# Performance work log

Hardware: AMD Instinct MI355X
Metric: run time of the kernel (lower is better)

## Reference

```python
import jax, jax.numpy as jnp
import numpy as np

N, P, C, S, H, CLS = 32, 16, 256, 128, 4, 3000
DH = C // H
EPS = 1e-5


def setup_inputs() -> dict:
    key = jax.random.key(0)
    ks = jax.random.split(key, 8)
    sh = (N, P, C, S)
    return {
        "t_f": jax.random.normal(ks[0], sh, jnp.float32),
        "t_s": jax.random.normal(ks[1], sh, jnp.float32),
        "t_l": jax.random.normal(ks[2], sh, jnp.float32),
        # grouped 1x1 conv weights, one [out_ch, in_ch] matrix per part
        "decay_w": jax.random.normal(ks[3], (P, C, 3 * C), jnp.float32) * 0.02,
        "qkv_w": jax.random.normal(ks[4], (P, 3 * C, C), jnp.float32) * 0.02,
        "out_w": jax.random.normal(ks[5], (P, C, C), jnp.float32) * 0.02,
        # per-part BatchNorm1d affine params
        "gamma": jnp.ones((P, C), jnp.float32),
        "beta": jnp.zeros((P, C), jnp.float32),
        # classifier fc: [in_planes, class_num] (broadcast over parts)
        "fc": jax.random.normal(ks[6], (C, CLS), jnp.float32) * 0.02,
    }


def reference(t_f, t_s, t_l, decay_w, qkv_w, out_w, gamma, beta, fc):
    n, p, c, s = t_f.shape
    h, dh = H, DH
    scale = dh ** -0.5

    # decay_c: grouped 1x1 conv, 3c -> c per part
    x_cat = jnp.concatenate([t_f, t_s, t_l], axis=2)            # [n,p,3c,s]
    t_all = jnp.einsum('npis,poi->npos', x_cat, decay_w)        # [n,p,c,s]

    # Attention.to_qkv: grouped 1x1 conv, c -> 3c per part
    qkv = jnp.einsum('npcs,pqc->npqs', t_all, qkv_w)            # [n,p,3c,s]
    qkv = qkv.reshape(n, p, 3, h, dh, s).transpose(2, 0, 3, 1, 4, 5)  # [3,n,h,p,dh,s]
    q, k, v = qkv[0], qkv[1], qkv[2]

    # frame-frame attention per (head, part): [n,h,p,s,s]
    dots = jnp.einsum('nhpcs,nhpct->nhpst', q, k) * scale
    attn = jax.nn.softmax(dots, axis=-1)

    o = jnp.einsum('nhpst,nhpct->nhpcs', attn, v)               # [n,h,p,dh,s]
    o = o.transpose(0, 2, 1, 3, 4).reshape(n, p, c, s)          # [n,p,c,s]
    o = jnp.einsum('npcs,poc->npos', o, out_w)                  # to_out grouped conv

    # residual + max over frames
    wpv = (o + t_all).max(axis=-1)                              # [n,p,c]

    # select_topk_part (topk_num == 1 forced by squeeze(2) in torch code):
    # argmax over frames of column-summed attention, gather that frame of t_f, sum heads
    idx = jnp.argmax(attn.sum(axis=-2), axis=-1)                # [n,h,p]
    ib = jnp.broadcast_to(idx[:, :, :, None, None], (n, h, p, c, 1))
    sel = jnp.take_along_axis(t_f[:, None], ib, axis=-1)[..., 0]  # [n,h,p,c]
    sel = sel.sum(axis=1)                                       # [n,p,c]

    # per-part BatchNorm1d in training mode (batch statistics over n)
    mean = wpv.mean(axis=0)                                     # [p,c]
    var = wpv.var(axis=0)                                       # biased, as torch BN
    pf = (wpv - mean) / jnp.sqrt(var + EPS) * gamma + beta      # [n,p,c]

    cls = jnp.einsum('npc,ck->npk', pf, fc)                     # [n,p,class_num]
    return cls, wpv.transpose(1, 0, 2), sel.transpose(1, 0, 2)
```

## Files before the change

### kernel.cpp

```cpp
#include <hip/hip_runtime.h>
#include <math.h>

#define N_ 32
#define P_ 16
#define C_ 256
#define S_ 128
#define H_ 4
#define CLS_ 3000

typedef __attribute__((ext_vector_type(4))) float f4v;
typedef __attribute__((ext_vector_type(4))) float f32x4;
typedef __attribute__((ext_vector_type(8))) short short8;
typedef __attribute__((ext_vector_type(4))) unsigned short us4;

__device__ __forceinline__ unsigned short f2bf(float x){
    unsigned u = __float_as_uint(x);
    u += 0x7fffu + ((u >> 16) & 1u);
    return (unsigned short)(u >> 16);
}
__device__ __forceinline__ float bf2f(unsigned short h){
    return __uint_as_float(((unsigned)h) << 16);
}

typedef __attribute__((address_space(1))) const unsigned int gu32_t;
typedef __attribute__((address_space(3))) unsigned int lu32_t;
__device__ __forceinline__ void gload16(const void* g, void* l){
    __builtin_amdgcn_global_load_lds((gu32_t*)g, (lu32_t*)l, 16, 0, 0);
}

__global__ void wsplit(const float* __restrict__ dw, const float* __restrict__ qw,
                       const float* __restrict__ ow,
                       unsigned short* __restrict__ wdh, unsigned short* __restrict__ wdl,
                       unsigned short* __restrict__ wqh, unsigned short* __restrict__ wql,
                       unsigned short* __restrict__ woh){
    int i = blockIdx.x * 256 + threadIdx.x;
    int stride = gridDim.x * 256;
    for (; i < 3145728; i += stride){
        float a = dw[i]; unsigned short h = f2bf(a);
        wdh[i] = h; wdl[i] = f2bf(a - bf2f(h));
        float b = qw[i]; unsigned short h2 = f2bf(b);
        wqh[i] = h2; wql[i] = f2bf(b - bf2f(h2));
        if (i < 1048576) woh[i] = f2bf(ow[i]);
    }
}

__global__ __launch_bounds__(256) void fct_kernel(const float* __restrict__ fc,
                                                  unsigned short* __restrict__ fcT){
    int n = blockIdx.x * 256 + threadIdx.x;
    if (n < CLS_){
        for (int c = 0; c < 256; ++c) fcT[(size_t)n * 256 + c] = f2bf(fc[(size_t)c * CLS_ + n]);
    } else {
        for (int c = 0; c < 256; ++c) fcT[(size_t)n * 256 + c] = 0;
    }
}

__global__ __launch_bounds__(256) void gemm0t(
    const float* __restrict__ t_f, const float* __restrict__ t_s,
    const float* __restrict__ t_l,
    const unsigned short* __restrict__ Whi, const unsigned short* __restrict__ Wlo,
    unsigned short* __restrict__ outH, unsigned short* __restrict__ outL,
    int n0, int cnp)
{
    __shared__ unsigned short sm[24576];
    float* Tf = (float*)sm;
    unsigned short* AhL = sm + 8192;
    unsigned short* AlL = sm + 12288;
    unsigned short* BhL = sm + 16384;
    unsigned short* BlL = sm + 20480;
    unsigned short* Ep  = sm;

    const int id = blockIdx.x;
    const int xcd = id & 7;
    const int r = id >> 3;
    const int ppl = r / (cnp * 2);
    const int rr = r % (cnp * 2);
    const int n_l = rr >> 1;
    const int o_t = rr & 1;
    const int p = xcd * 2 + ppl;
    const int np_l = n_l * 16 + p;
    const int o0 = o_t * 128;
    const size_t np_g = (size_t)(n0 + n_l) * 16 + p;

    const int tid = threadIdx.x;
    const int w = tid >> 6, l = tid & 63;
    const int lr = l & 15, lg = l >> 4;
    const int ws0 = (w & 1) * 64, wo0 = (w >> 1) * 64;
    const int s2 = tid & 127, khalf = tid >> 7;

    const unsigned short* Wp_h = Whi + ((size_t)p * 256 + o0) * 768;
    const unsigned short* Wp_l = Wlo + ((size_t)p * 256 + o0) * 768;

    f32x4 acc[4][4];
#pragma unroll
    for (int i = 0; i < 4; ++i)
#pragma unroll
        for (int j = 0; j < 4; ++j) acc[i][j] = (f32x4){0.f, 0.f, 0.f, 0.f};

    for (int k0 = 0; k0 < 768; k0 += 32){
        const int t = k0 >> 8;
        const float* src = (t == 0) ? t_f : ((t == 1) ? t_s : t_l);
        const float* xbase = src + (np_g * 256 + (k0 & 255)) * 128;
#pragma unroll
        for (int it = 0; it < 4; ++it){
            int lin = (w * 4 + it) * 64 + l;
            gload16(xbase + lin * 4, Tf + lin * 4);
        }
#pragma unroll
        for (int it = 0; it < 2; ++it){
            int lin = (w * 2 + it) * 64 + l;
            int row = lin >> 2, ch = lin & 3;
            int sk = ((ch ^ ((row >> 1) & 3)) << 3);
            gload16(Wp_h + (size_t)row * 768 + k0 + sk, BhL + lin * 8);
            gload16(Wp_l + (size_t)row * 768 + k0 + sk, BlL + lin * 8);
        }
        __syncthreads();
        {
            short8 h0, h1, l0, l1;
#pragma unroll
            for (int j = 0; j < 8; ++j){
                float v = Tf[(khalf * 16 + j) * 128 + s2];
                unsigned short hh = f2bf(v);
                h0[j] = (short)hh; l0[j] = (short)f2bf(v - bf2f(hh));
            }
#pragma unroll
            for (int j = 0; j < 8; ++j){
                float v = Tf[(khalf * 16 + 8 + j) * 128 + s2];
                unsigned short hh = f2bf(v);
                h1[j] = (short)hh; l1[j] = (short)f2bf(v - bf2f(hh));
            }
            int sb = (s2 >> 1) & 3;
            int c0 = (khalf * 2) ^ sb, c1 = (khalf * 2 + 1) ^ sb;
            *(short8*)(AhL + s2 * 32 + c0 * 8) = h0;
            *(short8*)(AhL + s2 * 32 + c1 * 8) = h1;
            *(short8*)(AlL + s2 * 32 + c0 * 8) = l0;
            *(short8*)(AlL + s2 * 32 + c1 * 8) = l1;
        }
        __syncthreads();
        short8 ah[4], al[4];
#pragma unroll
        for (int sf = 0; sf < 4; ++sf){
            int row = ws0 + sf * 16 + lr;
            int cof = (lg ^ ((row >> 1) & 3)) << 3;
            ah[sf] = *(const short8*)(AhL + row * 32 + cof);
            al[sf] = *(const short8*)(AlL + row * 32 + cof);
        }
#pragma unroll
        for (int of = 0; of < 4; ++of){
            int row = wo0 + of * 16 + lr;
            int cof = (lg ^ ((row >> 1) & 3)) << 3;
            short8 bh = *(const short8*)(BhL + row * 32 + cof);
            short8 bl = *(const short8*)(BlL + row * 32 + cof);
#pragma unroll
            for (int sf = 0; sf < 4; ++sf){
                acc[sf][of] = __builtin_amdgcn_mfma_f32_16x16x32_bf16(ah[sf], bh, acc[sf][of], 0, 0, 0);
                acc[sf][of] = __builtin_amdgcn_mfma_f32_16x16x32_bf16(ah[sf], bl, acc[sf][of], 0, 0, 0);
                acc[sf][of] = __builtin_amdgcn_mfma_f32_16x16x32_bf16(al[sf], bh, acc[sf][of], 0, 0, 0);
            }
        }
        __syncthreads();
    }

#pragma unroll
    for (int plane = 0; plane < 2; ++plane){
#pragma unroll
        for (int sf = 0; sf < 4; ++sf)
#pragma unroll
            for (int of = 0; of < 4; ++of){
                int col = wo0 + of * 16 + lr;
#pragma unroll
                for (int r2 = 0; r2 < 4; ++r2){
                    int row = ws0 + sf * 16 + lg * 4 + r2;
                    float v = acc[sf][of][r2];
                    unsigned short hh = f2bf(v);
                    unsigned short q = plane ? f2bf(v - bf2f(hh)) : hh;
                    Ep[row * 136 + col] = q;
                }
            }
        __syncthreads();
        unsigned short* dst = plane ? outL : outH;
#pragma unroll
        for (int it = 0; it < 8; ++it){
            int idx = tid + 256 * it;
            int row = idx >> 4, seg = (idx & 15) * 8;
            *(short8*)(dst + (size_t)np_l * 128 * 256 + (size_t)row * 256 + o0 + seg) =
                *(const short8*)(Ep + row * 136 + seg);
        }
        __syncthreads();
    }
}

template<int KEXT, int APITCH, int ND, int MODE, int OPITCH>
__global__ __launch_bounds__(256) void gemm3(
    const unsigned short* __restrict__ Ah_g, const unsigned short* __restrict__ Al_g,
    const unsigned short* __restrict__ Whi, const unsigned short* __restrict__ Wlo,
    const unsigned short* __restrict__ resH, const unsigned short* __restrict__ resL,
    unsigned short* __restrict__ outH, unsigned short* __restrict__ outL,
    float* __restrict__ outF, int n0, int cnp)
{
    constexpr int T3 = (MODE == 2) ? 0 : 1;
    constexpr int OB = ND / 128;
    __shared__ unsigned short sm[(T3 ? 4 : 2) * 128 * 64];
    unsigned short* AhL = sm;
    unsigned short* BhL = sm + 8192;
    unsigned short* AlL = T3 ? (sm + 16384) : sm;
    unsigned short* BlL = T3 ? (sm + 24576) : sm;
    unsigned short* Ep = sm;
    __shared__ float cmax[2][2][64];

    const int id = blockIdx.x;
    const int xcd = id & 7;
    const int r = id >> 3;
    const int ppl = r / (cnp * OB);
    const int rr = r % (cnp * OB);
    const int n_l = rr / OB;
    const int o_t = rr % OB;
    const int p = xcd * 2 + ppl;
    const int np_l = n_l * 16 + p;
    const int o0 = o_t * 128;

    const int tid = threadIdx.x;
    const int w = tid >> 6, l = tid & 63;
    const int lr = l & 15, lg = l >> 4;
    const int ws0 = (w & 1) * 64, wo0 = (w >> 1) * 64;
    const size_t aBase = (size_t)np_l * 128 * APITCH;
    const unsigned short* Wp_h = Whi + ((size_t)p * ND + o0) * KEXT;
    const unsigned short* Wp_l = T3 ? (Wlo + ((size_t)p * ND + o0) * KEXT) : Wp_h;

    f32x4 acc[4][4];
#pragma unroll
    for (int i = 0; i < 4; ++i)
#pragma unroll
        for (int j = 0; j < 4; ++j) acc[i][j] = (f32x4){0.f, 0.f, 0.f, 0.f};

    for (int k0 = 0; k0 < KEXT; k0 += 64){
#pragma unroll
        for (int it = 0; it < 4; ++it){
            int slot = w * 4 + it;
            int lin = slot * 64 + l;
            int row = lin >> 3, chnk = lin & 7;
            int sk = ((chnk ^ (row & 7)) << 3);
            unsigned short* ldst = sm + slot * 512;
            const unsigned short* ga = Ah_g + aBase + (size_t)row * APITCH + k0 + sk;
            gload16(ga, ldst);
            const unsigned short* gb = Wp_h + (size_t)row * KEXT + k0 + sk;
            gload16(gb, ldst + 8192);
            if (T3){
                gload16(Al_g + aBase + (size_t)row * APITCH + k0 + sk, ldst + 16384);
                gload16(Wp_l + (size_t)row * KEXT + k0 + sk, ldst + 24576);
            }
        }
        __syncthreads();
#pragma unroll
        for (int ks = 0; ks < 2; ++ks){
            short8 ah[4], al[4];
#pragma unroll
            for (int sf = 0; sf < 4; ++sf){
                int row = ws0 + sf * 16 + lr;
                int cof = ((ks * 4 + lg) ^ (row & 7)) << 3;
                ah[sf] = *(const short8*)(AhL + row * 64 + cof);
                if (T3) al[sf] = *(const short8*)(AlL + row * 64 + cof);
            }
#pragma unroll
            for (int of = 0; of < 4; ++of){
                int row = wo0 + of * 16 + lr;
                int cof = ((ks * 4 + lg) ^ (row & 7)) << 3;
                short8 bh = *(const short8*)(BhL + row * 64 + cof);
                short8 bl = bh;
                if (T3) bl = *(const short8*)(BlL + row * 64 + cof);
#pragma unroll
                for (int sf = 0; sf < 4; ++sf){
                    acc[sf][of] = __builtin_amdgcn_mfma_f32_16x16x32_bf16(ah[sf], bh, acc[sf][of], 0, 0, 0);
                    if (T3){
                        acc[sf][of] = __builtin_amdgcn_mfma_f32_16x16x32_bf16(ah[sf], bl, acc[sf][of], 0, 0, 0);
                        acc[sf][of] = __builtin_amdgcn_mfma_f32_16x16x32_bf16(al[sf], bh, acc[sf][of], 0, 0, 0);
                    }
                }
            }
        }
        __syncthreads();
    }

    if (MODE != 2){
#pragma unroll
        for (int plane = 0; plane < 2; ++plane){
#pragma unroll
            for (int sf = 0; sf < 4; ++sf)
#pragma unroll
                for (int of = 0; of < 4; ++of){
                    int col = wo0 + of * 16 + lr;
#pragma unroll
                    for (int r2 = 0; r2 < 4; ++r2){
                        int row = ws0 + sf * 16 + lg * 4 + r2;
                        float v = acc[sf][of][r2];
                        unsigned short hh = f2bf(v);
                        unsigned short q = plane ? f2bf(v - bf2f(hh)) : hh;
                        Ep[row * 136 + col] = q;
                    }
                }
            __syncthreads();
            unsigned short* dst = plane ? outL : outH;
#pragma unroll
            for (int it = 0; it < 8; ++it){
                int idx = tid + 256 * it;
                int row = idx >> 4, seg = (idx & 15) * 8;
                *(short8*)(dst + (size_t)np_l * 128 * OPITCH + (size_t)row * OPITCH + o0 + seg) =
                    *(const short8*)(Ep + row * 136 + seg);
            }
            __syncthreads();
        }
    } else {
        const int n_g = n0 + n_l;
#pragma unroll
        for (int of = 0; of < 4; ++of){
            int oc = o0 + wo0 + of * 16 + lr;
            float m = -INFINITY;
#pragma unroll
            for (int sf = 0; sf < 4; ++sf){
#pragma unroll
                for (int r2 = 0; r2 < 4; ++r2){
                    int s = ws0 + sf * 16 + lg * 4 + r2;
                    size_t ri = (size_t)np_l * 128 * 256 + (size_t)s * 256 + oc;
                    float v = acc[sf][of][r2] + bf2f(resH[ri]) + bf2f(resL[ri]);
                    m = fmaxf(m, v);
                }
            }
            m = fmaxf(m, __shfl_xor(m, 16));
            m = fmaxf(m, __shfl_xor(m, 32));
            if (l < 16) cmax[w >> 1][w & 1][of * 16 + l] = m;
        }
        __syncthreads();
        if (tid < 128){
            int oh = tid >> 6, col = tid & 63;
            float v = fmaxf(cmax[oh][0][col], cmax[oh][1][col]);
            outF[((size_t)p * N_ + n_g) * C_ + o0 + oh * 64 + col] = v;
        }
    }
}

__global__ __launch_bounds__(256) void attn3(unsigned short* __restrict__ qH,
                                             const unsigned short* __restrict__ qL,
                                             int* __restrict__ idxA, int n0, int cnp){
    __shared__ char smraw[17408 + 34816 + 2048];
    unsigned short* Vs = (unsigned short*)smraw;
    unsigned short* Pm = (unsigned short*)(smraw + 17408);
    float* csW = (float*)(smraw + 17408 + 34816);
    unsigned short* Ot = (unsigned short*)smraw;

    const int id = blockIdx.x;
    const int xcd = id & 7;
    const int r = id >> 3;
    const int ppl = r / (cnp * 4);
    const int rr = r % (cnp * 4);
    const int n_l = rr >> 2, h = rr & 3;
    const int p = xcd * 2 + ppl;
    const int np_l = n_l * 16 + p;
    const int tid = threadIdx.x, w = tid >> 6, l = tid & 63;
    const int lr = l & 15, lg = l >> 4;
    unsigned short* baseH = qH + (size_t)np_l * 128 * 768;
    const unsigned short* baseL = qL + (size_t)np_l * 128 * 768;

#pragma unroll
    for (int it = 0; it < 8; ++it){
        int idx = tid + 256 * it;
        int t = idx >> 4, d4 = (idx & 15) * 4;
        us4 v = *(const us4*)(baseH + (size_t)t * 768 + 512 + h * 64 + d4);
#pragma unroll
        for (int j = 0; j < 4; ++j) Vs[(d4 + j) * 136 + t] = v[j];
    }

    short8 qh[2][2], ql[2][2];
#pragma unroll
    for (int sf = 0; sf < 2; ++sf)
#pragma unroll
        for (int ks = 0; ks < 2; ++ks){
            size_t off = (size_t)(w * 32 + sf * 16 + lr) * 768 + h * 64 + ks * 32 + lg * 8;
            qh[sf][ks] = *(const short8*)(baseH + off);
            ql[sf][ks] = *(const short8*)(baseL + off);
        }

    f32x4 dacc[2][8];
#pragma unroll
    for (int i = 0; i < 2; ++i)
#pragma unroll
        for (int j = 0; j < 8; ++j) dacc[i][j] = (f32x4){0.f, 0.f, 0.f, 0.f};

#pragma unroll
    for (int tf = 0; tf < 8; ++tf){
#pragma unroll
        for (int ks = 0; ks < 2; ++ks){
            size_t off = (size_t)(tf * 16 + lr) * 768 + 256 + h * 64 + ks * 32 + lg * 8;
            short8 kh = *(const short8*)(baseH + off);
            short8 kl = *(const short8*)(baseL + off);
#pragma unroll
            for (int sf = 0; sf < 2; ++sf){
                dacc[sf][tf] = __builtin_amdgcn_mfma_f32_16x16x32_bf16(qh[sf][ks], kh, dacc[sf][tf], 0, 0, 0);
                dacc[sf][tf] = __builtin_amdgcn_mfma_f32_16x16x32_bf16(qh[sf][ks], kl, dacc[sf][tf], 0, 0, 0);
                dacc[sf][tf] = __builtin_amdgcn_mfma_f32_16x16x32_bf16(ql[sf][ks], kh, dacc[sf][tf], 0, 0, 0);
            }
        }
    }

    float csp[8];
#pragma unroll
    for (int tf = 0; tf < 8; ++tf) csp[tf] = 0.f;
#pragma unroll
    for (int sf = 0; sf < 2; ++sf){
#pragma unroll
        for (int r2 = 0; r2 < 4; ++r2){
            float m = -INFINITY;
#pragma unroll
            for (int tf = 0; tf < 8; ++tf) m = fmaxf(m, dacc[sf][tf][r2]);
            m = fmaxf(m, __shfl_xor(m, 1)); m = fmaxf(m, __shfl_xor(m, 2));
            m = fmaxf(m, __shfl_xor(m, 4)); m = fmaxf(m, __shfl_xor(m, 8));
            float e[8]; float sum = 0.f;
#pragma unroll
            for (int tf = 0; tf < 8; ++tf){
                e[tf] = __expf(0.125f * (dacc[sf][tf][r2] - m)); sum += e[tf];
            }
            sum += __shfl_xor(sum, 1); sum += __shfl_xor(sum, 2);
            sum += __shfl_xor(sum, 4); sum += __shfl_xor(sum, 8);
            float inv = 1.f / sum;
            int s = w * 32 + sf * 16 + lg * 4 + r2;
#pragma unroll
            for (int tf = 0; tf < 8; ++tf){
                float pv = e[tf] * inv;
                Pm[s * 136 + tf * 16 + lr] = f2bf(pv);
                csp[tf] += pv;
            }
        }
    }
#pragma unroll
    for (int tf = 0; tf < 8; ++tf){
        float v = csp[tf];
        v += __shfl_xor(v, 16); v += __shfl_xor(v, 32);
        if (l < 16) csW[w * 128 + tf * 16 + l] = v;
    }
    __syncthreads();

    f32x4 oacc[8];
#pragma unroll
    for (int i = 0; i < 8; ++i) oacc[i] = (f32x4){0.f, 0.f, 0.f, 0.f};
#pragma unroll
    for (int ks = 0; ks < 4; ++ks){
        short8 av = *(const short8*)(Vs + (w * 16 + lr) * 136 + ks * 32 + lg * 8);
#pragma unroll
        for (int sf = 0; sf < 8; ++sf){
            short8 bp = *(const short8*)(Pm + (sf * 16 + lr) * 136 + ks * 32 + lg * 8);
            oacc[sf] = __builtin_amdgcn_mfma_f32_16x16x32_bf16(av, bp, oacc[sf], 0, 0, 0);
        }
    }
    __syncthreads();

    if (tid < 64){
        float v0 = csW[tid] + csW[128 + tid] + csW[256 + tid] + csW[384 + tid];
        float v1 = csW[64 + tid] + csW[192 + tid] + csW[320 + tid] + csW[448 + tid];
        float bv; int bi;
        if (v1 > v0){ bv = v1; bi = 64 + tid; } else { bv = v0; bi = tid; }
#pragma unroll
        for (int msk = 1; msk <= 32; msk <<= 1){
            float ov = __shfl_xor(bv, msk); int oi = __shfl_xor(bi, msk);
            if (ov > bv || (ov == bv && oi < bi)){ bv = ov; bi = oi; }
        }
        if (tid == 0){ int n_g = n0 + n_l; idxA[(n_g * H_ + h) * P_ + p] = bi; }
    }

#pragma unroll
    for (int sf = 0; sf < 8; ++sf){
        int s = sf * 16 + lr;
#pragma unroll
        for (int r2 = 0; r2 < 4; ++r2) Ot[s * 72 + w * 16 + lg * 4 + r2] = f2bf(oacc[sf][r2]);
    }
    __syncthreads();
#pragma unroll
    for (int it = 0; it < 4; ++it){
        int idx = tid + 256 * it;
        int s = idx >> 3, d8 = (idx & 7) * 8;
        *(short8*)(baseH + (size_t)s * 768 + h * 64 + d8) = *(const short8*)(Ot + s * 72 + d8);
    }
}

__global__ void bn_stats(const float* __restrict__ wpvT,
                         const float* __restrict__ gamma,
                         const float* __restrict__ beta,
                         float* __restrict__ aArr, float* __restrict__ bArr)
{
    int i = blockIdx.x * blockDim.x + threadIdx.x;
    if (i >= P_ * C_) return;
    int p = i / C_, c = i % C_;
    const float* basep = wpvT + (size_t)p * N_ * C_ + c;
    float su = 0.f, s2 = 0.f;
    for (int n = 0; n < N_; ++n){
        float v = basep[n * C_];
        su += v; s2 += v * v;
    }
    float mean = su * (1.f / N_);
    float var = s2 * (1.f / N_) - mean * mean;
    float rstd = rsqrtf(var + 1e-5f);
    float a = gamma[i] * rstd;
    aArr[i] = a;
    bArr[i] = beta[i] - mean * a;
}

__global__ __launch_bounds__(256) void pf_kernel(const float* __restrict__ wpvT,
                                                 const float* __restrict__ aArr,
                                                 const float* __restrict__ bArr,
                                                 unsigned short* __restrict__ pfb){
    int m = blockIdx.x, c = threadIdx.x;
    int p = m >> 5;
    float v = wpvT[(size_t)m * 256 + c];
    pfb[(size_t)m * 256 + c] = f2bf(v * aArr[p * 256 + c] + bArr[p * 256 + c]);
}

__global__ __launch_bounds__(256) void gemmc(const unsigned short* __restrict__ pfb,
                                             const unsigned short* __restrict__ fcT,
                                             float* __restrict__ cls){
    __shared__ unsigned short sm[2 * 128 * 72];
    unsigned short* AhL = sm;
    unsigned short* BhL = sm + 128 * 72;

    const int tid = threadIdx.x;
    const int w = tid >> 6, l = tid & 63;
    const int lr = l & 15, lg = l >> 4;
    const int ws0 = (w & 1) * 64, wo0 = (w >> 1) * 64;
    const int o0 = blockIdx.x * 128;
    const int m0 = blockIdx.y * 128;

    f32x4 acc[4][4];
#pragma unroll
    for (int i = 0; i < 4; ++i)
#pragma unroll
        for (int j = 0; j < 4; ++j) acc[i][j] = (f32x4){0.f, 0.f, 0.f, 0.f};

    for (int k0 = 0; k0 < 256; k0 += 64){
#pragma unroll
        for (int it = 0; it < 4; ++it){
            int idx = tid + 256 * it;
            int s = idx >> 3, c8 = (idx & 7) * 8;
            *(short8*)(AhL + s * 72 + c8) = *(const short8*)(pfb + (size_t)(m0 + s) * 256 + k0 + c8);
            *(short8*)(BhL + s * 72 + c8) = *(const short8*)(fcT + (size_t)(o0 + s) * 256 + k0 + c8);
        }
        __syncthreads();
#pragma unroll
        for (int ks = 0; ks < 2; ++ks){
            short8 ah[4];
#pragma unroll
            for (int sf = 0; sf < 4; ++sf)
                ah[sf] = *(const short8*)(AhL + (ws0 + sf * 16 + lr) * 72 + ks * 32 + lg * 8);
#pragma unroll
            for (int of = 0; of < 4; ++of){
                short8 bh = *(const short8*)(BhL + (wo0 + of * 16 + lr) * 72 + ks * 32 + lg * 8);
#pragma unroll
                for (int sf = 0; sf < 4; ++sf)
                    acc[sf][of] = __builtin_amdgcn_mfma_f32_16x16x32_bf16(ah[sf], bh, acc[sf][of], 0, 0, 0);
            }
        }
        __syncthreads();
    }
#pragma unroll
    for (int sf = 0; sf < 4; ++sf)
#pragma unroll
        for (int of = 0; of < 4; ++of){
            int oc = o0 + wo0 + of * 16 + lr;
            if (oc < CLS_){
#pragma unroll
                for (int r2 = 0; r2 < 4; ++r2){
                    int m = m0 + ws0 + sf * 16 + lg * 4 + r2;
                    int n = m & 31, p = m >> 5;
                    cls[((size_t)n * 16 + p) * CLS_ + oc] = acc[sf][of][r2];
                }
            }
        }
}

__global__ void sel_kernel(const float* __restrict__ t_f,
                           const int* __restrict__ idxArr,
                           float* __restrict__ selT)
{
    const int np = blockIdx.x;
    const int n = np >> 4, p = np & 15;
    const int c = threadIdx.x;
    float acc = 0.f;
#pragma unroll
    for (int h = 0; h < H_; ++h){
        int s = idxArr[(n * H_ + h) * P_ + p];
        acc += t_f[((size_t)np * C_ + c) * S_ + s];
    }
    selT[((size_t)p * N_ + n) * C_ + c] = acc;
}

extern "C" void kernel_launch(void* const* d_in, const int* in_sizes, int n_in,
                              void* d_out, int out_size, void* d_ws, size_t ws_size,
                              hipStream_t stream)
{
    const float* t_f     = (const float*)d_in[0];
    const float* t_s     = (const float*)d_in[1];
    const float* t_l     = (const float*)d_in[2];
    const float* decay_w = (const float*)d_in[3];
    const float* qkv_w   = (const float*)d_in[4];
    const float* out_w   = (const float*)d_in[5];
    const float* gamma   = (const float*)d_in[6];
    const float* beta    = (const float*)d_in[7];
    const float* fc      = (const float*)d_in[8];
    float* out = (float*)d_out;

    const size_t WD = 3145728, WQ = 3145728, WO = 1048576;
    char* basep = (char*)d_ws;
    unsigned short* wdh = (unsigned short*)basep;
    unsigned short* wdl = wdh + WD;
    unsigned short* wqh = wdl + WD;
    unsigned short* wql = wqh + WQ;
    unsigned short* woh = wql + WQ;
    unsigned short* fcT = woh + WO;
    unsigned short* pfb = fcT + 3072 * 256;
    float* aArr = (float*)(pfb + 512 * 256);
    float* bArr = aArr + P_ * C_;
    int* idxA = (int*)(bArr + P_ * C_);
    char* big = (char*)(idxA + N_ * H_ * P_);
    size_t head = (size_t)(big - basep);
    size_t avail = (ws_size > head) ? (ws_size - head) : 0;
    const size_t per_n = (size_t)16 * 128 * (256 + 768) * 2 * 2;
    int cn = (int)(avail / per_n);
    if (cn < 1) cn = 1;
    if (cn > N_) cn = N_;
    int nch = (N_ + cn - 1) / cn;
    cn = (N_ + nch - 1) / nch;

    unsigned short* tH = (unsigned short*)big;
    unsigned short* tL = tH + (size_t)cn * 16 * 128 * 256;
    unsigned short* qH = tL + (size_t)cn * 16 * 128 * 256;
    unsigned short* qL = qH + (size_t)cn * 16 * 128 * 768;

    float* cls  = out;
    float* wpvT = out + (size_t)N_ * P_ * CLS_;
    float* selT = wpvT + (size_t)P_ * N_ * C_;

    wsplit<<<2048, 256, 0, stream>>>(decay_w, qkv_w, out_w, wdh, wdl, wqh, wql, woh);
    fct_kernel<<<12, 256, 0, stream>>>(fc, fcT);

    for (int n0 = 0; n0 < N_; n0 += cn){
        int c = (N_ - n0 < cn) ? (N_ - n0) : cn;
        int npg = c * 16;
        gemm0t<<<npg * 2, 256, 0, stream>>>(
            t_f, t_s, t_l, wdh, wdl, tH, tL, n0, c);
        gemm3<256, 256, 768, 1, 768><<<npg * 6, 256, 0, stream>>>(
            tH, tL, wqh, wql, nullptr, nullptr, qH, qL, nullptr, n0, c);
        attn3<<<c * 64, 256, 0, stream>>>(qH, qL, idxA, n0, c);
        gemm3<256, 768, 256, 2, 256><<<npg * 2, 256, 0, stream>>>(
            qH, qH, woh, woh, tH, tL, nullptr, nullptr, wpvT, n0, c);
    }
    bn_stats<<<(P_ * C_ + 255) / 256, 256, 0, stream>>>(wpvT, gamma, beta, aArr, bArr);
    pf_kernel<<<512, 256, 0, stream>>>(wpvT, aArr, bArr, pfb);
    gemmc<<<dim3(24, 4), 256, 0, stream>>>(pfb, fcT, cls);
    sel_kernel<<<N_ * P_, 256, 0, stream>>>(t_f, idxA, selT);
}
```

Before: 439.5 us.

## Retile decay GEMM over all outputs and halve K-step in gemm3

The first GEMM (decay conv) now has each block compute all 256 output channels for a 64-frame half, instead of 128 outputs over all 128 frames. Each fp32 input tile is therefore loaded and split into bf16 hi/lo once per block rather than twice, at the cost of re-reading the full weight slab per frame-half. The gemm3 kernel drops its K step from 64 to 32 with a matching swizzle, which cuts shared memory per block (likely to raise occupancy) but doubles the number of barriers per K loop.

```diff
diff --git a/kernel.cpp b/kernel.cpp
--- a/kernel.cpp
+++ b/kernel.cpp
@@ -63,10 +63,10 @@
 {
     __shared__ unsigned short sm[24576];
     float* Tf = (float*)sm;
-    unsigned short* AhL = sm + 8192;
-    unsigned short* AlL = sm + 12288;
-    unsigned short* BhL = sm + 16384;
-    unsigned short* BlL = sm + 20480;
+    unsigned short* AhL = sm + 4096;
+    unsigned short* AlL = sm + 6144;
+    unsigned short* BhL = sm + 8192;
+    unsigned short* BlL = sm + 16384;
     unsigned short* Ep  = sm;
 
     const int id = blockIdx.x;
@@ -75,20 +75,18 @@
     const int ppl = r / (cnp * 2);
     const int rr = r % (cnp * 2);
     const int n_l = rr >> 1;
-    const int o_t = rr & 1;
+    const int sh = rr & 1;
     const int p = xcd * 2 + ppl;
     const int np_l = n_l * 16 + p;
-    const int o0 = o_t * 128;
+    const int s0 = sh * 64;
     const size_t np_g = (size_t)(n0 + n_l) * 16 + p;
 
     const int tid = threadIdx.x;
     const int w = tid >> 6, l = tid & 63;
     const int lr = l & 15, lg = l >> 4;
-    const int ws0 = (w & 1) * 64, wo0 = (w >> 1) * 64;
-    const int s2 = tid & 127, khalf = tid >> 7;
-
-    const unsigned short* Wp_h = Whi + ((size_t)p * 256 + o0) * 768;
-    const unsigned short* Wp_l = Wlo + ((size_t)p * 256 + o0) * 768;
+
+    const unsigned short* Wp_h = Whi + (size_t)p * 256 * 768;
+    const unsigned short* Wp_l = Wlo + (size_t)p * 256 * 768;
 
     f32x4 acc[4][4];
 #pragma unroll
@@ -99,57 +97,52 @@
     for (int k0 = 0; k0 < 768; k0 += 32){
         const int t = k0 >> 8;
         const float* src = (t == 0) ? t_f : ((t == 1) ? t_s : t_l);
-        const float* xbase = src + (np_g * 256 + (k0 & 255)) * 128;
+        const float* xbase = src + (np_g * 256 + (k0 & 255)) * 128 + s0;
+#pragma unroll
+        for (int it = 0; it < 2; ++it){
+            int slot = w * 2 + it;
+            int lin = slot * 64 + l;
+            int k = lin >> 4, choff = lin & 15;
+            gload16(xbase + (size_t)k * 128 + choff * 4, (unsigned short*)Tf + slot * 512);
+        }
 #pragma unroll
         for (int it = 0; it < 4; ++it){
-            int lin = (w * 4 + it) * 64 + l;
-            gload16(xbase + lin * 4, Tf + lin * 4);
-        }
-#pragma unroll
-        for (int it = 0; it < 2; ++it){
-            int lin = (w * 2 + it) * 64 + l;
+            int slot = w * 4 + it;
+            int lin = slot * 64 + l;
             int row = lin >> 2, ch = lin & 3;
             int sk = ((ch ^ ((row >> 1) & 3)) << 3);
-            gload16(Wp_h + (size_t)row * 768 + k0 + sk, BhL + lin * 8);
-            gload16(Wp_l + (size_t)row * 768 + k0 + sk, BlL + lin * 8);
+            gload16(Wp_h + (size_t)row * 768 + k0 + sk, BhL + slot * 512);
+            gload16(Wp_l + (size_t)row * 768 + k0 + sk, BlL + slot * 512);
         }
         __syncthreads();
         {
-            short8 h0, h1, l0, l1;
+            const int s = tid & 63, kq = tid >> 6;
+            short8 hi, lo;
 #pragma unroll
             for (int j = 0; j < 8; ++j){
-                float v = Tf[(khalf * 16 + j) * 128 + s2];
+                float v = Tf[(kq * 8 + j) * 64 + s];
                 unsigned short hh = f2bf(v);
-                h0[j] = (short)hh; l0[j] = (short)f2bf(v - bf2f(hh));
-            }
-#pragma unroll
-            for (int j = 0; j < 8; ++j){
-                float v = Tf[(khalf * 16 + 8 + j) * 128 + s2];
-                unsigned short hh = f2bf(v);
-                h1[j] = (short)hh; l1[j] = (short)f2bf(v - bf2f(hh));
-            }
-            int sb = (s2 >> 1) & 3;
-            int c0 = (khalf * 2) ^ sb, c1 = (khalf * 2 + 1) ^ sb;
-            *(short8*)(AhL + s2 * 32 + c0 * 8) = h0;
-            *(short8*)(AhL + s2 * 32 + c1 * 8) = h1;
-            *(short8*)(AlL + s2 * 32 + c0 * 8) = l0;
-            *(short8*)(AlL + s2 * 32 + c1 * 8) = l1;
+                hi[j] = (short)hh; lo[j] = (short)f2bf(v - bf2f(hh));
+            }
+            int c = kq ^ ((s >> 1) & 3);
+            *(short8*)(AhL + s * 32 + c * 8) = hi;
+            *(short8*)(AlL + s * 32 + c * 8) = lo;
         }
         __syncthreads();
         short8 ah[4], al[4];
 #pragma unroll
         for (int sf = 0; sf < 4; ++sf){
-            int row = ws0 + sf * 16 + lr;
+            int row = sf * 16 + lr;
             int cof = (lg ^ ((row >> 1) & 3)) << 3;
             ah[sf] = *(const short8*)(AhL + row * 32 + cof);
             al[sf] = *(const short8*)(AlL + row * 32 + cof);
         }
 #pragma unroll
         for (int of = 0; of < 4; ++of){
-            int row = wo0 + of * 16 + lr;
-            int cof = (lg ^ ((row >> 1) & 3)) << 3;
-            short8 bh = *(const short8*)(BhL + row * 32 + cof);
-            short8 bl = *(const short8*)(BlL + row * 32 + cof);
+            int brow = w * 64 + of * 16 + lr;
+            int cof = (lg ^ ((brow >> 1) & 3)) << 3;
+            short8 bh = *(const short8*)(BhL + brow * 32 + cof);
+            short8 bl = *(const short8*)(BlL + brow * 32 + cof);
 #pragma unroll
             for (int sf = 0; sf < 4; ++sf){
                 acc[sf][of] = __builtin_amdgcn_mfma_f32_16x16x32_bf16(ah[sf], bh, acc[sf][of], 0, 0, 0);
@@ -166,14 +159,14 @@
         for (int sf = 0; sf < 4; ++sf)
 #pragma unroll
             for (int of = 0; of < 4; ++of){
-                int col = wo0 + of * 16 + lr;
+                int col = w * 64 + of * 16 + lr;
 #pragma unroll
                 for (int r2 = 0; r2 < 4; ++r2){
-                    int row = ws0 + sf * 16 + lg * 4 + r2;
+                    int row = sf * 16 + lg * 4 + r2;
                     float v = acc[sf][of][r2];
                     unsigned short hh = f2bf(v);
                     unsigned short q = plane ? f2bf(v - bf2f(hh)) : hh;
-                    Ep[row * 136 + col] = q;
+                    Ep[row * 264 + col] = q;
                 }
             }
         __syncthreads();
@@ -181,9 +174,9 @@
 #pragma unroll
         for (int it = 0; it < 8; ++it){
             int idx = tid + 256 * it;
-            int row = idx >> 4, seg = (idx & 15) * 8;
-            *(short8*)(dst + (size_t)np_l * 128 * 256 + (size_t)row * 256 + o0 + seg) =
-                *(const short8*)(Ep + row * 136 + seg);
+            int row = idx >> 5, sgi = (idx & 31) * 8;
+            *(short8*)(dst + (size_t)np_l * 128 * 256 + (size_t)(s0 + row) * 256 + sgi) =
+                *(const short8*)(Ep + row * 264 + sgi);
         }
         __syncthreads();
     }
@@ -199,11 +192,11 @@
 {
     constexpr int T3 = (MODE == 2) ? 0 : 1;
     constexpr int OB = ND / 128;
-    __shared__ unsigned short sm[(T3 ? 4 : 2) * 128 * 64];
+    __shared__ unsigned short sm[T3 ? 17408 : 8192];
     unsigned short* AhL = sm;
-    unsigned short* BhL = sm + 8192;
-    unsigned short* AlL = T3 ? (sm + 16384) : sm;
-    unsigned short* BlL = T3 ? (sm + 24576) : sm;
+    unsigned short* BhL = sm + 4096;
+    unsigned short* AlL = T3 ? (sm + 8192) : sm;
+    unsigned short* BlL = T3 ? (sm + 12288) : sm;
     unsigned short* Ep = sm;
     __shared__ float cmax[2][2][64];
 
@@ -232,48 +225,42 @@
 #pragma unroll
         for (int j = 0; j < 4; ++j) acc[i][j] = (f32x4){0.f, 0.f, 0.f, 0.f};
 
-    for (int k0 = 0; k0 < KEXT; k0 += 64){
-#pragma unroll
-        for (int it = 0; it < 4; ++it){
-            int slot = w * 4 + it;
+    for (int k0 = 0; k0 < KEXT; k0 += 32){
+#pragma unroll
+        for (int it = 0; it < 2; ++it){
+            int slot = w * 2 + it;
             int lin = slot * 64 + l;
-            int row = lin >> 3, chnk = lin & 7;
-            int sk = ((chnk ^ (row & 7)) << 3);
-            unsigned short* ldst = sm + slot * 512;
-            const unsigned short* ga = Ah_g + aBase + (size_t)row * APITCH + k0 + sk;
-            gload16(ga, ldst);
-            const unsigned short* gb = Wp_h + (size_t)row * KEXT + k0 + sk;
-            gload16(gb, ldst + 8192);
+            int row = lin >> 2, ch = lin & 3;
+            int sk = ((ch ^ ((row >> 1) & 3)) << 3);
+            gload16(Ah_g + aBase + (size_t)row * APITCH + k0 + sk, AhL + slot * 512);
+            gload16(Wp_h + (size_t)row * KEXT + k0 + sk, BhL + slot * 512);
             if (T3){
-                gload16(Al_g + aBase + (size_t)row * APITCH + k0 + sk, ldst + 16384);
-                gload16(Wp_l + (size_t)row * KEXT + k0 + sk, ldst + 24576);
-            }
-        }
-        __syncthreads();
-#pragma unroll
-        for (int ks = 0; ks < 2; ++ks){
-            short8 ah[4], al[4];
+                gload16(Al_g + aBase + (size_t)row * APITCH + k0 + sk, AlL + slot * 512);
+                gload16(Wp_l + (size_t)row * KEXT + k0 + sk, BlL + slot * 512);
+            }
+        }
+        __syncthreads();
+        short8 ah[4], al[4];
+#pragma unroll
+        for (int sf = 0; sf < 4; ++sf){
+            int row = ws0 + sf * 16 + lr;
+            int cof = (lg ^ ((row >> 1) & 3)) << 3;
+            ah[sf] = *(const short8*)(AhL + row * 32 + cof);
+            if (T3) al[sf] = *(const short8*)(AlL + row * 32 + cof);
+        }
+#pragma unroll
+        for (int of = 0; of < 4; ++of){
+            int row = wo0 + of * 16 + lr;
+            int cof = (lg ^ ((row >> 1) & 3)) << 3;
+            short8 bh = *(const short8*)(BhL + row * 32 + cof);
+            short8 bl = bh;
+            if (T3) bl = *(const short8*)(BlL + row * 32 + cof);
 #pragma unroll
             for (int sf = 0; sf < 4; ++sf){
-                int row = ws0 + sf * 16 + lr;
-                int cof = ((ks * 4 + lg) ^ (row & 7)) << 3;
-                ah[sf] = *(const short8*)(AhL + row * 64 + cof);
-                if (T3) al[sf] = *(const short8*)(AlL + row * 64 + cof);
-            }
-#pragma unroll
-            for (int of = 0; of < 4; ++of){
-                int row = wo0 + of * 16 + lr;
-                int cof = ((ks * 4 + lg) ^ (row & 7)) << 3;
-                short8 bh = *(const short8*)(BhL + row * 64 + cof);
-                short8 bl = bh;
-                if (T3) bl = *(const short8*)(BlL + row * 64 + cof);
-#pragma unroll
-                for (int sf = 0; sf < 4; ++sf){
-                    acc[sf][of] = __builtin_amdgcn_mfma_f32_16x16x32_bf16(ah[sf], bh, acc[sf][of], 0, 0, 0);
-                    if (T3){
-                        acc[sf][of] = __builtin_amdgcn_mfma_f32_16x16x32_bf16(ah[sf], bl, acc[sf][of], 0, 0, 0);
-                        acc[sf][of] = __builtin_amdgcn_mfma_f32_16x16x32_bf16(al[sf], bh, acc[sf][of], 0, 0, 0);
-                    }
+                acc[sf][of] = __builtin_amdgcn_mfma_f32_16x16x32_bf16(ah[sf], bh, acc[sf][of], 0, 0, 0);
+                if (T3){
+                    acc[sf][of] = __builtin_amdgcn_mfma_f32_16x16x32_bf16(ah[sf], bl, acc[sf][of], 0, 0, 0);
+                    acc[sf][of] = __builtin_amdgcn_mfma_f32_16x16x32_bf16(al[sf], bh, acc[sf][of], 0, 0, 0);
                 }
             }
         }
```

New measurement: 444.3 us. No clear change (+1.1%).

## Double-buffer LDS tiles in gemm3 with K-step 32 prefetch

Applied to the files above, without the earlier changes.

Replaces the single-buffered 64-wide K tile in gemm3 with two LDS buffers of 32-wide K tiles. The next tile's global-to-LDS loads are issued before the current tile's MFMAs, so load latency can overlap compute, and one barrier per iteration is dropped. The swizzle is adapted to the 32-element row pitch. In exchange the loop runs twice as many iterations with less MFMA work per barrier, and the epilogue still reuses the same shared array.

```diff
diff --git a/kernel.cpp b/kernel.cpp
--- a/kernel.cpp
+++ b/kernel.cpp
@@ -199,11 +199,8 @@
 {
     constexpr int T3 = (MODE == 2) ? 0 : 1;
     constexpr int OB = ND / 128;
-    __shared__ unsigned short sm[(T3 ? 4 : 2) * 128 * 64];
-    unsigned short* AhL = sm;
-    unsigned short* BhL = sm + 8192;
-    unsigned short* AlL = T3 ? (sm + 16384) : sm;
-    unsigned short* BlL = T3 ? (sm + 24576) : sm;
+    constexpr int BUFSH = T3 ? 16384 : 8192;
+    __shared__ unsigned short sm[2 * BUFSH];
     unsigned short* Ep = sm;
     __shared__ float cmax[2][2][64];
 
@@ -232,52 +229,58 @@
 #pragma unroll
         for (int j = 0; j < 4; ++j) acc[i][j] = (f32x4){0.f, 0.f, 0.f, 0.f};
 
-    for (int k0 = 0; k0 < KEXT; k0 += 64){
-#pragma unroll
-        for (int it = 0; it < 4; ++it){
-            int slot = w * 4 + it;
+    auto STAGE = [&](int bsel, int k0){
+        unsigned short* B0 = sm + bsel * BUFSH;
+#pragma unroll
+        for (int it = 0; it < 2; ++it){
+            int slot = w * 2 + it;
             int lin = slot * 64 + l;
-            int row = lin >> 3, chnk = lin & 7;
-            int sk = ((chnk ^ (row & 7)) << 3);
-            unsigned short* ldst = sm + slot * 512;
-            const unsigned short* ga = Ah_g + aBase + (size_t)row * APITCH + k0 + sk;
-            gload16(ga, ldst);
-            const unsigned short* gb = Wp_h + (size_t)row * KEXT + k0 + sk;
-            gload16(gb, ldst + 8192);
+            int row = lin >> 2, ch = lin & 3;
+            int sk = ((ch ^ ((row >> 1) & 3)) << 3);
+            gload16(Ah_g + aBase + (size_t)row * APITCH + k0 + sk, B0 + slot * 512);
+            gload16(Wp_h + (size_t)row * KEXT + k0 + sk, B0 + 4096 + slot * 512);
             if (T3){
-                gload16(Al_g + aBase + (size_t)row * APITCH + k0 + sk, ldst + 16384);
-                gload16(Wp_l + (size_t)row * KEXT + k0 + sk, ldst + 24576);
-            }
-        }
-        __syncthreads();
-#pragma unroll
-        for (int ks = 0; ks < 2; ++ks){
-            short8 ah[4], al[4];
+                gload16(Al_g + aBase + (size_t)row * APITCH + k0 + sk, B0 + 8192 + slot * 512);
+                gload16(Wp_l + (size_t)row * KEXT + k0 + sk, B0 + 12288 + slot * 512);
+            }
+        }
+    };
+
+    STAGE(0, 0);
+    __syncthreads();
+    int cur = 0;
+    for (int k0 = 0; k0 < KEXT; k0 += 32){
+        if (k0 + 32 < KEXT) STAGE(cur ^ 1, k0 + 32);
+        unsigned short* AhL = sm + cur * BUFSH;
+        unsigned short* BhL = AhL + 4096;
+        unsigned short* AlL = T3 ? (AhL + 8192) : AhL;
+        unsigned short* BlL = T3 ? (AhL + 12288) : AhL;
+        short8 ah[4], al[4];
+#pragma unroll
+        for (int sf = 0; sf < 4; ++sf){
+            int row = ws0 + sf * 16 + lr;
+            int cof = (lg ^ ((row >> 1) & 3)) << 3;
+            ah[sf] = *(const short8*)(AhL + row * 32 + cof);
+            if (T3) al[sf] = *(const short8*)(AlL + row * 32 + cof);
+        }
+#pragma unroll
+        for (int of = 0; of < 4; ++of){
+            int row = wo0 + of * 16 + lr;
+            int cof = (lg ^ ((row >> 1) & 3)) << 3;
+            short8 bh = *(const short8*)(BhL + row * 32 + cof);
+            short8 bl = bh;
+            if (T3) bl = *(const short8*)(BlL + row * 32 + cof);
 #pragma unroll
             for (int sf = 0; sf < 4; ++sf){
-                int row = ws0 + sf * 16 + lr;
-                int cof = ((ks * 4 + lg) ^ (row & 7)) << 3;
-                ah[sf] = *(const short8*)(AhL + row * 64 + cof);
-                if (T3) al[sf] = *(const short8*)(AlL + row * 64 + cof);
-            }
-#pragma unroll
-            for (int of = 0; of < 4; ++of){
-                int row = wo0 + of * 16 + lr;
-                int cof = ((ks * 4 + lg) ^ (row & 7)) << 3;
-                short8 bh = *(const short8*)(BhL + row * 64 + cof);
-                short8 bl = bh;
-                if (T3) bl = *(const short8*)(BlL + row * 64 + cof);
-#pragma unroll
-                for (int sf = 0; sf < 4; ++sf){
-                    acc[sf][of] = __builtin_amdgcn_mfma_f32_16x16x32_bf16(ah[sf], bh, acc[sf][of], 0, 0, 0);
-                    if (T3){
-                        acc[sf][of] = __builtin_amdgcn_mfma_f32_16x16x32_bf16(ah[sf], bl, acc[sf][of], 0, 0, 0);
-                        acc[sf][of] = __builtin_amdgcn_mfma_f32_16x16x32_bf16(al[sf], bh, acc[sf][of], 0, 0, 0);
-                    }
+                acc[sf][of] = __builtin_amdgcn_mfma_f32_16x16x32_bf16(ah[sf], bh, acc[sf][of], 0, 0, 0);
+                if (T3){
+                    acc[sf][of] = __builtin_amdgcn_mfma_f32_16x16x32_bf16(ah[sf], bl, acc[sf][of], 0, 0, 0);
+                    acc[sf][of] = __builtin_amdgcn_mfma_f32_16x16x32_bf16(al[sf], bh, acc[sf][of], 0, 0, 0);
                 }
             }
         }
         __syncthreads();
+        cur ^= 1;
     }
 
     if (MODE != 2){
```

New measurement: 448.1 us. Within noise of the previous version (+2.0%).
